# Kernel optimization log

Measured on AMD Instinct MI355X. Metric: run time of the kernel, lower is better.

## Reference

```python
import jax, jax.numpy as jnp
import numpy as np

DIM = 2048
N_HEADS = 32
N_KV_HEADS = 8
HEAD_DIM = 64
REPEATS = N_HEADS // N_KV_HEADS
SLIDING_WINDOW = 1024
EPS = 1e-6
B, T = 2, 2048


def _alibi_slopes(n):
    # n_heads=32 is a power of 2
    r = 2.0 ** (-8.0 / n)
    return jnp.asarray([r ** i for i in range(n)], dtype=jnp.float32)


def _rms_norm(x, w, eps):
    # RMSNorm over the last (flattened heads*head_dim) axis
    var = jnp.mean(x * x, axis=-1, keepdims=True)
    return x * jax.lax.rsqrt(var + eps) * w


def setup_inputs() -> dict:
    key = jax.random.key(0)
    ks = jax.random.split(key, 6)
    s = 0.02
    return {
        "x": jax.random.normal(ks[0], (B, T, DIM), jnp.float32),
        "wq": jax.random.normal(ks[1], (N_HEADS * HEAD_DIM, DIM), jnp.float32) * s,
        "wk": jax.random.normal(ks[2], (N_KV_HEADS * HEAD_DIM, DIM), jnp.float32) * s,
        "wv": jax.random.normal(ks[3], (N_KV_HEADS * HEAD_DIM, DIM), jnp.float32) * s,
        "wo": jax.random.normal(ks[4], (DIM, N_HEADS * HEAD_DIM), jnp.float32) * s,
        "q_norm_w": jnp.ones((N_HEADS * HEAD_DIM,), jnp.float32),
        "k_norm_w": jnp.ones((N_KV_HEADS * HEAD_DIM,), jnp.float32),
    }


def reference(x, wq, wk, wv, wo, q_norm_w, k_norm_w):
    bsz, seqlen, _ = x.shape
    xq = _rms_norm(x @ wq.T, q_norm_w, EPS)
    xk = _rms_norm(x @ wk.T, k_norm_w, EPS)
    xv = x @ wv.T
    xq = xq.reshape(bsz, seqlen, N_HEADS, HEAD_DIM).transpose(0, 2, 1, 3)  # b h t d
    xk = xk.reshape(bsz, seqlen, N_KV_HEADS, HEAD_DIM).transpose(0, 2, 1, 3)
    xv = xv.reshape(bsz, seqlen, N_KV_HEADS, HEAD_DIM).transpose(0, 2, 1, 3)
    # GQA: repeat_interleave kv heads
    xk = jnp.repeat(xk, REPEATS, axis=1)
    xv = jnp.repeat(xv, REPEATS, axis=1)

    pos = jnp.arange(seqlen)
    dist = pos[None, :] - pos[:, None]                     # [t,s] = s - t (<=0 on causal side)
    slopes = _alibi_slopes(N_HEADS)
    alibi = slopes[:, None, None] * dist.astype(jnp.float32)  # [h,t,s]
    allowed = (dist <= 0) & (dist >= -SLIDING_WINDOW)      # causal + sliding window
    bias = jnp.where(allowed[None], alibi, -jnp.inf)       # [h,t,s]

    scale = 1.0 / jnp.sqrt(jnp.asarray(HEAD_DIM, jnp.float32))
    scores = jnp.einsum("bhtd,bhsd->bhts", xq, xk) * scale + bias[None]
    attn = jax.nn.softmax(scores, axis=-1)
    out = jnp.einsum("bhts,bhsd->bhtd", attn, xv)          # [b,h,t,d]
    out = out.transpose(0, 2, 1, 3).reshape(bsz, seqlen, N_HEADS * HEAD_DIM)
    return out @ wo.T
```

## Files before the change

### kernel.cpp

```cpp
#include <hip/hip_runtime.h>


typedef _Float16 f16;
typedef __attribute__((ext_vector_type(8))) _Float16 f16x8;
typedef __attribute__((ext_vector_type(4))) _Float16 f16x4;
typedef __attribute__((ext_vector_type(2))) _Float16 f16x2;
typedef __attribute__((ext_vector_type(4))) float f32x4;

#define T_ 2048
#define NH 32
#define NKV 8
#define HD 64
#define WINDOW 1024
#define EPS_ 1e-6f
#define LOG2E 1.44269504088896340736f
#define LDQKV 3072

__device__ inline void async16(void* lds, const void* g) {
  __builtin_amdgcn_global_load_lds(
      (const __attribute__((address_space(1))) unsigned int*)g,
      (__attribute__((address_space(3))) unsigned int*)lds, 16, 0, 0);
}

struct CvtArgs {
  const float* src[5];
  f16* dst[5];
  int n4[5];
};
__global__ __launch_bounds__(256) void cvt_multi(CvtArgs a) {
  const int seg = blockIdx.y;
  const float* in = a.src[seg];
  f16* out = a.dst[seg];
  const int n4 = a.n4[seg];
  for (int i = blockIdx.x * blockDim.x + threadIdx.x; i < n4;
       i += gridDim.x * blockDim.x) {
    float4 v = ((const float4*)in)[i];
    f16x4 o;
    o[0] = (f16)v.x; o[1] = (f16)v.y; o[2] = (f16)v.z; o[3] = (f16)v.w;
    ((f16x4*)out)[i] = o;
  }
}

#define DSRD(p, off) (*(const f16x8*)((p) + (off)))

__global__ __launch_bounds__(512, 1) void gemm_nt192(const f16* __restrict__ A,
                                                     const f16* __restrict__ B,
                                                     f16* __restrict__ C) {
  constexpr int K = 2048, ldc = 3072;
  extern __shared__ char smem[];
  f16* sA = (f16*)smem;
  f16* sB = (f16*)(smem + 65536);

  const int gx = gridDim.x;
  const int nwg = gx * gridDim.y;
  int bid = blockIdx.y * gx + blockIdx.x;
  bid = (bid & 7) * (nwg >> 3) + (bid >> 3);
  const int m0 = (bid / gx) * 256;
  const int n0 = (bid % gx) * 192;

  const int tid = threadIdx.x;
  const int lane = tid & 63;
  const int wave = tid >> 6;
  const int quad = lane >> 4, l16 = lane & 15;
  const int wm = wave >> 2, wn = wave & 3;

  const int srow = tid >> 3;
  const int sgr = (((tid & 7) ^ (srow & 7))) * 8;
  const f16* gA = A + (size_t)(m0 + srow) * K + sgr;
  const f16* gB = B + (size_t)(n0 + srow) * K + sgr;
  const size_t r64 = (size_t)64 * K;

  const char* cA = (const char*)sA;
  const char* cB = (const char*)sB;
  const int xm = (l16 & 7) << 4;
  const int xk0 = (quad * 16) ^ xm;
  const int xk1 = (64 + quad * 16) ^ xm;
  const int abase = (wm * 128 + l16) * 128;
  const int bbase = (wn * 48 + l16) * 128;

  f32x4 acc[8][3] = {};
  const int nt = K >> 6;

#pragma unroll
  for (int a = 0; a < 4; ++a)
    async16(sA + a * 4096 + tid * 8, gA + (size_t)a * r64);
#pragma unroll
  for (int rb = 0; rb < 3; ++rb)
    async16(sB + rb * 4096 + tid * 8, gB + (size_t)rb * r64);
  asm volatile("s_waitcnt vmcnt(0)" ::: "memory");
  __builtin_amdgcn_s_barrier();

  for (int t = 0; t < nt; ++t) {
    const int bufoA = (t & 1) << 15;
    const int bufoB = (t & 1) * 24576;
    f16* sAn = sA + (((t & 1) ^ 1) << 14);
    f16* sBn = sB + ((t & 1) ^ 1) * 12288;
    const bool st = (t + 1 < nt);
    const size_t gk = (size_t)(t + 1) * 64;

    f16x8 af[4], bf[3][2];

    auto ldA = [&](int mh, int xk) {
#pragma unroll
      for (int i = 0; i < 4; ++i)
        af[i] = DSRD(cA, bufoA + abase + mh * 8192 + i * 2048 + xk);
    };
    auto mm = [&](int mh, int kc) {
      __builtin_amdgcn_s_barrier();
      asm volatile("s_waitcnt lgkmcnt(0)" ::: "memory");
      __builtin_amdgcn_sched_barrier(0);
      __builtin_amdgcn_s_setprio(1);
#pragma unroll
      for (int i = 0; i < 4; ++i)
#pragma unroll
        for (int j = 0; j < 3; ++j)
          acc[mh * 4 + i][j] = __builtin_amdgcn_mfma_f32_16x16x32_f16(
              af[i], bf[j][kc], acc[mh * 4 + i][j], 0, 0, 0);
      __builtin_amdgcn_s_setprio(0);
    };

    ldA(0, xk0);
#pragma unroll
    for (int j = 0; j < 3; ++j) {
      bf[j][0] = DSRD(cB, bufoB + bbase + j * 2048 + xk0);
      bf[j][1] = DSRD(cB, bufoB + bbase + j * 2048 + xk1);
    }
    if (st) {
#pragma unroll
      for (int a = 0; a < 4; ++a)
        async16(sAn + a * 4096 + tid * 8, gA + a * r64 + gk);
    }
    mm(0, 0);
    __builtin_amdgcn_s_barrier();

    ldA(0, xk1);
    if (st) {
#pragma unroll
      for (int rb = 0; rb < 3; ++rb)
        async16(sBn + rb * 4096 + tid * 8, gB + rb * r64 + gk);
    }
    mm(0, 1);
    __builtin_amdgcn_s_barrier();

    ldA(1, xk0);
    mm(1, 0);
    __builtin_amdgcn_s_barrier();

    ldA(1, xk1);
    mm(1, 1);
    if (st) asm volatile("s_waitcnt vmcnt(0)" ::: "memory");
    __builtin_amdgcn_s_barrier();
  }

#pragma unroll
  for (int im = 0; im < 8; ++im) {
    const int row0 = m0 + wm * 128 + im * 16 + quad * 4;
#pragma unroll
    for (int j = 0; j < 3; ++j) {
      const int col = n0 + wn * 48 + j * 16 + l16;
#pragma unroll
      for (int r = 0; r < 4; ++r)
        C[(size_t)(row0 + r) * ldc + col] = (f16)acc[im][j][r];
    }
  }
}

template <int BN>
__global__ __launch_bounds__(512, 2) void gemm_nt8(const f16* __restrict__ A,
                                                   const f16* __restrict__ B,
                                                   void* __restrict__ C,
                                                   int M, int N, int K, int ldc,
                                                   int out_f32) {
  constexpr int WN = BN / 4;
  constexpr int JN = WN / 32;
  constexpr int RB = BN / 64;
  constexpr int BUFB = BN * 128;
  extern __shared__ char smem[];
  f16* sA = (f16*)smem;
  f16* sB = (f16*)(smem + 65536);

  const int gx = gridDim.x;
  const int nwg = gx * gridDim.y;
  int bid = blockIdx.y * gx + blockIdx.x;
  if (!(nwg & 7)) bid = (bid & 7) * (nwg >> 3) + (bid >> 3);
  const int m0 = (bid / gx) * 256;
  const int n0 = (bid % gx) * BN;

  const int tid = threadIdx.x;
  const int lane = tid & 63;
  const int wave = tid >> 6;
  const int quad = lane >> 4, l16 = lane & 15;
  const int wm = wave >> 2, wn = wave & 3;

  const int srow = tid >> 3;
  const int sgr = (((tid & 7) ^ (srow & 7))) * 8;
  const f16* gA = A + (size_t)(m0 + srow) * K + sgr;
  const f16* gB = B + (size_t)(n0 + srow) * K + sgr;
  const size_t r64 = (size_t)64 * K;

  const char* cA = (const char*)sA;
  const char* cB = (const char*)sB;
  const int xm = (l16 & 7) << 4;
  const int xk0 = (quad * 16) ^ xm;
  const int xk1 = (64 + quad * 16) ^ xm;
  const int abase = (wm * 128 + l16) * 128;
  const int bbase = (wn * WN + l16) * 128;

  f32x4 acc[8][2 * JN] = {};
  const int nt = K >> 6;

#pragma unroll
  for (int a = 0; a < 4; ++a)
    async16(sA + a * 4096 + tid * 8, gA + (size_t)a * r64);
#pragma unroll
  for (int rb = 0; rb < RB; ++rb)
    async16(sB + rb * 4096 + tid * 8, gB + (size_t)rb * r64);
  asm volatile("s_waitcnt vmcnt(0)" ::: "memory");
  __builtin_amdgcn_s_barrier();

  for (int t = 0; t < nt; ++t) {
    const int bufoA = (t & 1) << 15;
    const int bufoB = (t & 1) * BUFB;
    f16* sAn = sA + (((t & 1) ^ 1) << 14);
    f16* sBn = sB + ((t & 1) ^ 1) * (BUFB / 2);
    const bool st = (t + 1 < nt);
    const size_t gk = (size_t)(t + 1) * 64;

    f16x8 af[4][2], bf[JN][2];

    auto ldA = [&](int mh) {
#pragma unroll
      for (int i = 0; i < 4; ++i) {
        af[i][0] = DSRD(cA, bufoA + abase + mh * 8192 + i * 2048 + xk0);
        af[i][1] = DSRD(cA, bufoA + abase + mh * 8192 + i * 2048 + xk1);
      }
    };
    auto ldB = [&](int nh) {
#pragma unroll
      for (int j = 0; j < JN; ++j) {
        bf[j][0] = DSRD(cB, bufoB + bbase + nh * (WN / 2) * 128 + j * 2048 + xk0);
        bf[j][1] = DSRD(cB, bufoB + bbase + nh * (WN / 2) * 128 + j * 2048 + xk1);
      }
    };
    auto mm = [&](int mh, int nh) {
      __builtin_amdgcn_s_barrier();
      asm volatile("s_waitcnt lgkmcnt(0)" ::: "memory");
      __builtin_amdgcn_sched_barrier(0);
      __builtin_amdgcn_s_setprio(1);
#pragma unroll
      for (int i = 0; i < 4; ++i) {
#pragma unroll
        for (int j = 0; j < JN; ++j) {
          acc[mh * 4 + i][nh * JN + j] = __builtin_amdgcn_mfma_f32_16x16x32_f16(
              af[i][0], bf[j][0], acc[mh * 4 + i][nh * JN + j], 0, 0, 0);
          acc[mh * 4 + i][nh * JN + j] = __builtin_amdgcn_mfma_f32_16x16x32_f16(
              af[i][1], bf[j][1], acc[mh * 4 + i][nh * JN + j], 0, 0, 0);
        }
      }
      __builtin_amdgcn_s_setprio(0);
    };

    ldA(0); ldB(0);
    if (st) {
#pragma unroll
      for (int a = 0; a < 4; ++a)
        async16(sAn + a * 4096 + tid * 8, gA + a * r64 + gk);
#pragma unroll
      for (int rb = 0; rb < RB; ++rb)
        async16(sBn + rb * 4096 + tid * 8, gB + rb * r64 + gk);
    }
    mm(0, 0);
    __builtin_amdgcn_s_barrier();

    ldB(1);
    mm(0, 1);
    __builtin_amdgcn_s_barrier();

    ldA(1); ldB(0);
    mm(1, 0);
    __builtin_amdgcn_s_barrier();

    ldB(1);
    mm(1, 1);
    if (st) asm volatile("s_waitcnt vmcnt(0)" ::: "memory");
    __builtin_amdgcn_s_barrier();
  }

#pragma unroll
  for (int im = 0; im < 8; ++im) {
    const int row0 = m0 + wm * 128 + im * 16 + quad * 4;
#pragma unroll
    for (int jn = 0; jn < 2 * JN; ++jn) {
      const int col = n0 + wn * WN + jn * 16 + l16;
#pragma unroll
      for (int r = 0; r < 4; ++r) {
        const float v = acc[im][jn][r];
        if (out_f32) ((float*)C)[(size_t)(row0 + r) * ldc + col] = v;
        else         ((f16*)C)[(size_t)(row0 + r) * ldc + col] = (f16)v;
      }
    }
  }
}

__global__ __launch_bounds__(256) void rmsnorm2(f16* __restrict__ xqkv,
                                                const float* __restrict__ qw,
                                                const float* __restrict__ kw) {
  __shared__ float red[4];
  const int which = blockIdx.y;
  const int tid = threadIdx.x;

  auto block_sum = [&](float ss) -> float {
#pragma unroll
    for (int off = 32; off > 0; off >>= 1) ss += __shfl_down(ss, off);
    if ((tid & 63) == 0) red[tid >> 6] = ss;
    __syncthreads();
    return red[0] + red[1] + red[2] + red[3];
  };

  if (which == 0) {
    f16* p = xqkv + (size_t)blockIdx.x * LDQKV;
    f16x8 v = ((const f16x8*)p)[tid];
    float f[8];
    float ss = 0.f;
#pragma unroll
    for (int j = 0; j < 8; ++j) { f[j] = (float)v[j]; ss += f[j] * f[j]; }
    const float scale = rsqrtf(block_sum(ss) / 2048.0f + EPS_);
    const float4 w0 = ((const float4*)qw)[tid * 2];
    const float4 w1 = ((const float4*)qw)[tid * 2 + 1];
    f16x8 o;
    o[0] = (f16)(f[0] * scale * w0.x); o[1] = (f16)(f[1] * scale * w0.y);
    o[2] = (f16)(f[2] * scale * w0.z); o[3] = (f16)(f[3] * scale * w0.w);
    o[4] = (f16)(f[4] * scale * w1.x); o[5] = (f16)(f[5] * scale * w1.y);
    o[6] = (f16)(f[6] * scale * w1.z); o[7] = (f16)(f[7] * scale * w1.w);
    ((f16x8*)p)[tid] = o;
  } else {
    f16* p = xqkv + (size_t)blockIdx.x * LDQKV + 2048;
    f16x2 v = ((const f16x2*)p)[tid];
    const float f0 = (float)v[0], f1 = (float)v[1];
    const float scale = rsqrtf(block_sum(f0 * f0 + f1 * f1) / 512.0f + EPS_);
    const float2 w = ((const float2*)kw)[tid];
    f16x2 o;
    o[0] = (f16)(f0 * scale * w.x);
    o[1] = (f16)(f1 * scale * w.y);
    ((f16x2*)p)[tid] = o;
  }
}

__global__ __launch_bounds__(256) void kvfrag(const f16* __restrict__ xqkv,
                                              f16* __restrict__ Kf,
                                              f16* __restrict__ Vf) {
  __shared__ f16 Lk[64][72];
  __shared__ f16 Lv[64][72];
  const int kt = blockIdx.x;
  const int b = blockIdx.y >> 3, kh = blockIdx.y & 7;
  const int t0 = kt * 64;
  const int tid = threadIdx.x;
  const int r = tid >> 3, c = (tid & 7) * 8;
#pragma unroll
  for (int rp = 0; rp < 2; ++rp) {
    const int rr = r + rp * 32;
    const f16* src = xqkv + (size_t)(b * T_ + t0 + rr) * LDQKV + kh * 64 + c;
    *(f16x8*)(&Lk[rr][c]) = *(const f16x8*)(src + 2048);
    *(f16x8*)(&Lv[rr][c]) = *(const f16x8*)(src + 2560);
  }
  __syncthreads();
  const size_t obase = ((size_t)(b * 8 + kh) * 32 + kt) * 4096;
#pragma unroll
  for (int cc0 = 0; cc0 < 2; ++cc0) {
    const int cc = tid + cc0 * 256;
    const int nb = cc >> 7, kc = (cc >> 6) & 1, ln = cc & 63;
    const int qd = ln >> 4, s16 = ln & 15;
    *(f16x8*)(Kf + obase + cc * 8) = *(const f16x8*)(&Lk[nb * 16 + s16][kc * 32 + qd * 8]);
    f16x8 o;
#pragma unroll
    for (int j = 0; j < 8; ++j) o[j] = Lv[kc * 32 + qd * 8 + j][nb * 16 + s16];
    *(f16x8*)(Vf + obase + cc * 8) = o;
  }
}

__global__ __launch_bounds__(256, 4) void attn(const f16* __restrict__ Q,
                                               const f16* __restrict__ Kf,
                                               const f16* __restrict__ Vf,
                                               f16* __restrict__ O) {
  constexpr int LDW = 72;
  __shared__ f16 Qs[128 * LDW];
  __shared__ float Lx[4][2][16];

  const int qt2 = 15 - blockIdx.x;
  const int h = blockIdx.y, b = blockIdx.z;
  const int kh = h >> 2;
  const int q0 = qt2 * 128;
  const int tid = threadIdx.x;
  const int lane = tid & 63, wave = tid >> 6;
  const int quad = lane >> 4, l16 = lane & 15;
  const float scale2 = 0.125f * LOG2E;
  const float slope2 = exp2f(-0.25f * (float)h) * LOG2E;
  const float M2 = 10.0f;

  const int sr = tid >> 3, sc = (tid & 7) * 8;

#pragma unroll
  for (int rp = 0; rp < 4; ++rp) {
    const int rr = sr + rp * 32;
    *(f16x8*)(Qs + rr * LDW + sc) =
        *(const f16x8*)(Q + (size_t)(b * T_ + q0 + rr) * LDQKV + h * HD + sc);
  }
  __syncthreads();
  f16x8 qa[2], qb[2];
#pragma unroll
  for (int kc = 0; kc < 2; ++kc) {
    qa[kc] = *(const f16x8*)(Qs + (wave * 32 + l16) * LDW + kc * 32 + quad * 8);
    qb[kc] = *(const f16x8*)(Qs + (wave * 32 + 16 + l16) * LDW + kc * 32 + quad * 8);
  }
  f16* PsA = Qs + (wave * 32) * LDW;
  f16* PsB = Qs + (wave * 32 + 16) * LDW;

  f32x4 o0[4] = {}, o1[4] = {};
  float lsA = 0.f, lsB = 0.f;

  const int kt_lo = (q0 >= WINDOW) ? ((q0 - WINDOW) >> 6) : 0;
  const int kt_hi = (q0 + 127) >> 6;
  const int gA0 = q0 + wave * 32;
  const int gB0 = gA0 + 16;
  const int qA = gA0 + l16;
  const int qB = qA + 16;
  const f16* kfb = Kf + (size_t)(b * 8 + kh) * 131072 + lane * 8;
  const f16* vfb = Vf + (size_t)(b * 8 + kh) * 131072 + lane * 8;

  float sr4[4];
#pragma unroll
  for (int r = 0; r < 4; ++r) sr4[r] = slope2 * (float)r;
  float baseA = slope2 * (float)(kt_lo * 64 + quad * 4 - qA) - M2;
  float baseB = slope2 * (float)(kt_lo * 64 + quad * 4 - qB) - M2;
  const float bstep = slope2 * 64.0f;
  const float b16 = slope2 * 16.0f;

  for (int kt = kt_lo; kt <= kt_hi; ++kt) {
    const int k0 = kt * 64;
    const f16* kp = kfb + kt * 4096;
    const f16* vp = vfb + kt * 4096;
    const bool maskA = (k0 + 63 > gA0) || (k0 + WINDOW < gA0 + 15);
    const bool maskB = (k0 + 63 > gB0) || (k0 + WINDOW < gB0 + 15);

    float bnbA = baseA, bnbB = baseB;
#pragma unroll
    for (int nb = 0; nb < 4; ++nb) {
      const f16x8 k0f = *(const f16x8*)(kp + (nb * 2) * 512);
      const f16x8 k1f = *(const f16x8*)(kp + (nb * 2 + 1) * 512);
      f32x4 a = {0.f, 0.f, 0.f, 0.f};
      a = __builtin_amdgcn_mfma_f32_16x16x32_f16(k0f, qa[0], a, 0, 0, 0);
      a = __builtin_amdgcn_mfma_f32_16x16x32_f16(k1f, qa[1], a, 0, 0, 0);
      f32x4 c = {0.f, 0.f, 0.f, 0.f};
      c = __builtin_amdgcn_mfma_f32_16x16x32_f16(k0f, qb[0], c, 0, 0, 0);
      c = __builtin_amdgcn_mfma_f32_16x16x32_f16(k1f, qb[1], c, 0, 0, 0);

      f16x4 pkA, pkB;
#pragma unroll
      for (int r = 0; r < 4; ++r) {
        const int key = k0 + nb * 16 + quad * 4 + r;
        float vA = fmaf(a[r], scale2, bnbA + sr4[r]);
        if (maskA) {
          const int dist = key - qA;
          if (dist > 0 || dist < -WINDOW) vA = -1e30f;
        }
        const float pA = __builtin_amdgcn_exp2f(vA);
        lsA += pA;
        pkA[r] = (f16)pA;
        float vB = fmaf(c[r], scale2, bnbB + sr4[r]);
        if (maskB) {
          const int dist = key - qB;
          if (dist > 0 || dist < -WINDOW) vB = -1e30f;
        }
        const float pB = __builtin_amdgcn_exp2f(vB);
        lsB += pB;
        pkB[r] = (f16)pB;
      }
      *(f16x4*)(PsA + l16 * LDW + nb * 16 + quad * 4) = pkA;
      *(f16x4*)(PsB + l16 * LDW + nb * 16 + quad * 4) = pkB;
      bnbA += b16; bnbB += b16;
    }
    baseA += bstep; baseB += bstep;

    const f16x8 paA0 = *(const f16x8*)(PsA + l16 * LDW + quad * 8);
    const f16x8 paA1 = *(const f16x8*)(PsA + l16 * LDW + 32 + quad * 8);
    const f16x8 paB0 = *(const f16x8*)(PsB + l16 * LDW + quad * 8);
    const f16x8 paB1 = *(const f16x8*)(PsB + l16 * LDW + 32 + quad * 8);
#pragma unroll
    for (int nb = 0; nb < 4; ++nb) {
      const f16x8 v0 = *(const f16x8*)(vp + (nb * 2) * 512);
      const f16x8 v1 = *(const f16x8*)(vp + (nb * 2 + 1) * 512);
      o0[nb] = __builtin_amdgcn_mfma_f32_16x16x32_f16(paA0, v0, o0[nb], 0, 0, 0);
      o0[nb] = __builtin_amdgcn_mfma_f32_16x16x32_f16(paA1, v1, o0[nb], 0, 0, 0);
      o1[nb] = __builtin_amdgcn_mfma_f32_16x16x32_f16(paB0, v0, o1[nb], 0, 0, 0);
      o1[nb] = __builtin_amdgcn_mfma_f32_16x16x32_f16(paB1, v1, o1[nb], 0, 0, 0);
    }
  }

  lsA += __shfl_xor(lsA, 16);
  lsA += __shfl_xor(lsA, 32);
  lsB += __shfl_xor(lsB, 16);
  lsB += __shfl_xor(lsB, 32);
  if (quad == 0) { Lx[wave][0][l16] = lsA; Lx[wave][1][l16] = lsB; }
  float rlA[4], rlB[4];
#pragma unroll
  for (int r = 0; r < 4; ++r) {
    rlA[r] = 1.0f / Lx[wave][0][quad * 4 + r];
    rlB[r] = 1.0f / Lx[wave][1][quad * 4 + r];
  }

#pragma unroll
  for (int r = 0; r < 4; ++r) {
    const int qrA = q0 + wave * 32 + quad * 4 + r;
#pragma unroll
    for (int nb = 0; nb < 4; ++nb) {
      O[(size_t)(b * T_ + qrA) * (NH * HD) + h * HD + nb * 16 + l16] =
          (f16)(o0[nb][r] * rlA[r]);
      O[(size_t)(b * T_ + qrA + 16) * (NH * HD) + h * HD + nb * 16 + l16] =
          (f16)(o1[nb][r] * rlB[r]);
    }
  }
}

extern "C" void kernel_launch(void* const* d_in, const int* in_sizes, int n_in,
                              void* d_out, int out_size, void* d_ws, size_t ws_size,
                              hipStream_t stream) {
  const float* x  = (const float*)d_in[0];
  const float* wq = (const float*)d_in[1];
  const float* wk = (const float*)d_in[2];
  const float* wv = (const float*)d_in[3];
  const float* wo = (const float*)d_in[4];
  const float* qw = (const float*)d_in[5];
  const float* kw = (const float*)d_in[6];
  float* out = (float*)d_out;

  char* ws = (char*)d_ws;
  size_t off = 0;
  auto carve = [&](size_t bytes) -> char* {
    char* p = ws + off;
    off += (bytes + 255) & ~(size_t)255;
    return p;
  };
  f16* xh    = (f16*)carve((size_t)4096 * 2048 * 2);
  f16* wqkvh = (f16*)carve((size_t)3072 * 2048 * 2);
  f16* woh   = (f16*)carve((size_t)2048 * 2048 * 2);
  f16* xqkv  = (f16*)carve((size_t)4096 * 3072 * 2);
  f16* Kf = wqkvh;
  f16* Vf = wqkvh + (size_t)16 * 131072;
  f16* ao = xh;

  static bool attr_done = false;
  if (!attr_done) {
    (void)hipFuncSetAttribute((const void*)gemm_nt192,
                              hipFuncAttributeMaxDynamicSharedMemorySize,
                              114688);
    (void)hipFuncSetAttribute((const void*)gemm_nt8<128>,
                              hipFuncAttributeMaxDynamicSharedMemorySize,
                              98304);
    attr_done = true;
  }

  CvtArgs ca;
  ca.src[0] = x;  ca.dst[0] = xh;                            ca.n4[0] = (4096 * 2048) / 4;
  ca.src[1] = wq; ca.dst[1] = wqkvh;                         ca.n4[1] = (2048 * 2048) / 4;
  ca.src[2] = wk; ca.dst[2] = wqkvh + (size_t)2048 * 2048;   ca.n4[2] = (512 * 2048) / 4;
  ca.src[3] = wv; ca.dst[3] = wqkvh + (size_t)2560 * 2048;   ca.n4[3] = (512 * 2048) / 4;
  ca.src[4] = wo; ca.dst[4] = woh;                           ca.n4[4] = (2048 * 2048) / 4;
  cvt_multi<<<dim3(1024, 5), 256, 0, stream>>>(ca);

  gemm_nt192<<<dim3(16, 16), 512, 114688, stream>>>(xh, wqkvh, xqkv);
  rmsnorm2<<<dim3(4096, 2), 256, 0, stream>>>(xqkv, qw, kw);
  kvfrag<<<dim3(32, 16), 256, 0, stream>>>(xqkv, Kf, Vf);
  attn<<<dim3(16, 32, 2), 256, 0, stream>>>(xqkv, Kf, Vf, ao);
  gemm_nt8<128><<<dim3(16, 16), 512, 98304, stream>>>(ao, woh, out, 4096, 2048, 2048, 2048, 1);
}
```

Baseline: 289.8 us.

## Drop per-phase barriers and setprio in GEMM main loops, one barrier per K-tile

Rewrites the K-loop of both GEMM kernels. The four barrier-separated phases with explicit lgkmcnt waits, sched_barrier and setprio are replaced by a single prefetch issue followed by a compiler-scheduled load-and-MFMA block, with one barrier per K-tile. The aim is to cut barrier and wait stalls and let the compiler interleave LDS reads with MFMAs. The risk is that the compiler's schedule overlaps worse, register pressure rises from holding all B fragments at once, and warps drift apart without the lockstep phases.

```diff
diff --git a/kernel.cpp b/kernel.cpp
--- a/kernel.cpp
+++ b/kernel.cpp
@@ -93,63 +93,49 @@
   for (int t = 0; t < nt; ++t) {
     const int bufoA = (t & 1) << 15;
     const int bufoB = (t & 1) * 24576;
-    f16* sAn = sA + (((t & 1) ^ 1) << 14);
-    f16* sBn = sB + ((t & 1) ^ 1) * 12288;
     const bool st = (t + 1 < nt);
-    const size_t gk = (size_t)(t + 1) * 64;
-
-    f16x8 af[4], bf[3][2];
-
-    auto ldA = [&](int mh, int xk) {
-#pragma unroll
-      for (int i = 0; i < 4; ++i)
-        af[i] = DSRD(cA, bufoA + abase + mh * 8192 + i * 2048 + xk);
-    };
-    auto mm = [&](int mh, int kc) {
-      __builtin_amdgcn_s_barrier();
-      asm volatile("s_waitcnt lgkmcnt(0)" ::: "memory");
-      __builtin_amdgcn_sched_barrier(0);
-      __builtin_amdgcn_s_setprio(1);
-#pragma unroll
-      for (int i = 0; i < 4; ++i)
-#pragma unroll
-        for (int j = 0; j < 3; ++j)
-          acc[mh * 4 + i][j] = __builtin_amdgcn_mfma_f32_16x16x32_f16(
-              af[i], bf[j][kc], acc[mh * 4 + i][j], 0, 0, 0);
-      __builtin_amdgcn_s_setprio(0);
-    };
-
-    ldA(0, xk0);
+
+    if (st) {
+      f16* sAn = sA + (((t & 1) ^ 1) << 14);
+      f16* sBn = sB + ((t & 1) ^ 1) * 12288;
+      const size_t gk = (size_t)(t + 1) * 64;
+#pragma unroll
+      for (int a = 0; a < 4; ++a)
+        async16(sAn + a * 4096 + tid * 8, gA + a * r64 + gk);
+#pragma unroll
+      for (int rb = 0; rb < 3; ++rb)
+        async16(sBn + rb * 4096 + tid * 8, gB + rb * r64 + gk);
+    }
+
+    f16x8 bf[3][2];
 #pragma unroll
     for (int j = 0; j < 3; ++j) {
       bf[j][0] = DSRD(cB, bufoB + bbase + j * 2048 + xk0);
       bf[j][1] = DSRD(cB, bufoB + bbase + j * 2048 + xk1);
     }
+#pragma unroll
+    for (int mh = 0; mh < 2; ++mh) {
+      f16x8 a0[4], a1[4];
+#pragma unroll
+      for (int i = 0; i < 4; ++i) {
+        a0[i] = DSRD(cA, bufoA + abase + mh * 8192 + i * 2048 + xk0);
+        a1[i] = DSRD(cA, bufoA + abase + mh * 8192 + i * 2048 + xk1);
+      }
+#pragma unroll
+      for (int i = 0; i < 4; ++i)
+#pragma unroll
+        for (int j = 0; j < 3; ++j) {
+          acc[mh * 4 + i][j] = __builtin_amdgcn_mfma_f32_16x16x32_f16(
+              a0[i], bf[j][0], acc[mh * 4 + i][j], 0, 0, 0);
+          acc[mh * 4 + i][j] = __builtin_amdgcn_mfma_f32_16x16x32_f16(
+              a1[i], bf[j][1], acc[mh * 4 + i][j], 0, 0, 0);
+        }
+    }
+
     if (st) {
-#pragma unroll
-      for (int a = 0; a < 4; ++a)
-        async16(sAn + a * 4096 + tid * 8, gA + a * r64 + gk);
-    }
-    mm(0, 0);
-    __builtin_amdgcn_s_barrier();
-
-    ldA(0, xk1);
-    if (st) {
-#pragma unroll
-      for (int rb = 0; rb < 3; ++rb)
-        async16(sBn + rb * 4096 + tid * 8, gB + rb * r64 + gk);
-    }
-    mm(0, 1);
-    __builtin_amdgcn_s_barrier();
-
-    ldA(1, xk0);
-    mm(1, 0);
-    __builtin_amdgcn_s_barrier();
-
-    ldA(1, xk1);
-    mm(1, 1);
-    if (st) asm volatile("s_waitcnt vmcnt(0)" ::: "memory");
-    __builtin_amdgcn_s_barrier();
+      asm volatile("s_waitcnt vmcnt(0)" ::: "memory");
+      __builtin_amdgcn_s_barrier();
+    }
   }
 
 #pragma unroll
@@ -221,47 +207,12 @@
   for (int t = 0; t < nt; ++t) {
     const int bufoA = (t & 1) << 15;
     const int bufoB = (t & 1) * BUFB;
-    f16* sAn = sA + (((t & 1) ^ 1) << 14);
-    f16* sBn = sB + ((t & 1) ^ 1) * (BUFB / 2);
     const bool st = (t + 1 < nt);
-    const size_t gk = (size_t)(t + 1) * 64;
-
-    f16x8 af[4][2], bf[JN][2];
-
-    auto ldA = [&](int mh) {
-#pragma unroll
-      for (int i = 0; i < 4; ++i) {
-        af[i][0] = DSRD(cA, bufoA + abase + mh * 8192 + i * 2048 + xk0);
-        af[i][1] = DSRD(cA, bufoA + abase + mh * 8192 + i * 2048 + xk1);
-      }
-    };
-    auto ldB = [&](int nh) {
-#pragma unroll
-      for (int j = 0; j < JN; ++j) {
-        bf[j][0] = DSRD(cB, bufoB + bbase + nh * (WN / 2) * 128 + j * 2048 + xk0);
-        bf[j][1] = DSRD(cB, bufoB + bbase + nh * (WN / 2) * 128 + j * 2048 + xk1);
-      }
-    };
-    auto mm = [&](int mh, int nh) {
-      __builtin_amdgcn_s_barrier();
-      asm volatile("s_waitcnt lgkmcnt(0)" ::: "memory");
-      __builtin_amdgcn_sched_barrier(0);
-      __builtin_amdgcn_s_setprio(1);
-#pragma unroll
-      for (int i = 0; i < 4; ++i) {
-#pragma unroll
-        for (int j = 0; j < JN; ++j) {
-          acc[mh * 4 + i][nh * JN + j] = __builtin_amdgcn_mfma_f32_16x16x32_f16(
-              af[i][0], bf[j][0], acc[mh * 4 + i][nh * JN + j], 0, 0, 0);
-          acc[mh * 4 + i][nh * JN + j] = __builtin_amdgcn_mfma_f32_16x16x32_f16(
-              af[i][1], bf[j][1], acc[mh * 4 + i][nh * JN + j], 0, 0, 0);
-        }
-      }
-      __builtin_amdgcn_s_setprio(0);
-    };
-
-    ldA(0); ldB(0);
+
     if (st) {
+      f16* sAn = sA + (((t & 1) ^ 1) << 14);
+      f16* sBn = sB + ((t & 1) ^ 1) * (BUFB / 2);
+      const size_t gk = (size_t)(t + 1) * 64;
 #pragma unroll
       for (int a = 0; a < 4; ++a)
         async16(sAn + a * 4096 + tid * 8, gA + a * r64 + gk);
@@ -269,21 +220,40 @@
       for (int rb = 0; rb < RB; ++rb)
         async16(sBn + rb * 4096 + tid * 8, gB + rb * r64 + gk);
     }
-    mm(0, 0);
-    __builtin_amdgcn_s_barrier();
-
-    ldB(1);
-    mm(0, 1);
-    __builtin_amdgcn_s_barrier();
-
-    ldA(1); ldB(0);
-    mm(1, 0);
-    __builtin_amdgcn_s_barrier();
-
-    ldB(1);
-    mm(1, 1);
-    if (st) asm volatile("s_waitcnt vmcnt(0)" ::: "memory");
-    __builtin_amdgcn_s_barrier();
+
+    f16x8 bf[2 * JN][2];
+#pragma unroll
+    for (int nh = 0; nh < 2; ++nh)
+#pragma unroll
+      for (int j = 0; j < JN; ++j) {
+        bf[nh * JN + j][0] =
+            DSRD(cB, bufoB + bbase + nh * (WN / 2) * 128 + j * 2048 + xk0);
+        bf[nh * JN + j][1] =
+            DSRD(cB, bufoB + bbase + nh * (WN / 2) * 128 + j * 2048 + xk1);
+      }
+#pragma unroll
+    for (int mh = 0; mh < 2; ++mh) {
+      f16x8 a0[4], a1[4];
+#pragma unroll
+      for (int i = 0; i < 4; ++i) {
+        a0[i] = DSRD(cA, bufoA + abase + mh * 8192 + i * 2048 + xk0);
+        a1[i] = DSRD(cA, bufoA + abase + mh * 8192 + i * 2048 + xk1);
+      }
+#pragma unroll
+      for (int i = 0; i < 4; ++i)
+#pragma unroll
+        for (int j = 0; j < 2 * JN; ++j) {
+          acc[mh * 4 + i][j] = __builtin_amdgcn_mfma_f32_16x16x32_f16(
+              a0[i], bf[j][0], acc[mh * 4 + i][j], 0, 0, 0);
+          acc[mh * 4 + i][j] = __builtin_amdgcn_mfma_f32_16x16x32_f16(
+              a1[i], bf[j][1], acc[mh * 4 + i][j], 0, 0, 0);
+        }
+    }
+
+    if (st) {
+      asm volatile("s_waitcnt vmcnt(0)" ::: "memory");
+      __builtin_amdgcn_s_barrier();
+    }
   }
 
 #pragma unroll
```

Result: faster. 281.7 us (median of 3 runs) (-2.8%).
